# Kernel optimization log

Hardware: AMD Instinct MI355X
Metric: run time of the kernel (lower is better)

## Reference

```python
import jax, jax.numpy as jnp
import numpy as np

SOFTPLUS_MIN = 1e-10
SOFTPLUS_MAX = 10000.0


def setup_inputs() -> dict:
    key = jax.random.key(0)
    k1, k2, k3, k4, k5 = jax.random.split(key, 5)
    N, M, D, S = 8192, 4096, 512, 16
    x = jax.random.normal(k1, (N, D), dtype=jnp.float32)
    y = jax.random.normal(k2, (M, D), dtype=jnp.float32)
    sample_x = jax.random.uniform(k3, (N, S), dtype=jnp.float32)
    sample_y = jax.random.uniform(k4, (M, S), dtype=jnp.float32)
    scale = jax.random.uniform(k5, (S,), dtype=jnp.float32)
    cutoff = jnp.full((1,), 0.1, dtype=jnp.float32)
    phi = jnp.ones((1,), dtype=jnp.float32)
    return {"x": x, "y": y, "sample_x": sample_x, "sample_y": sample_y,
            "scale": scale, "cutoff": cutoff, "phi": phi}


def reference(x, y, sample_x, sample_y, scale, cutoff, phi):
    # pairwise squared distances via norm trick: d[i,j] = |x_i|^2 + |y_j|^2 - 2 x_i.y_j
    sq_x = jnp.sum(x * x, axis=-1, keepdims=True)            # [N,1]
    sq_y = jnp.sum(y * y, axis=-1, keepdims=True).T          # [1,M]
    dot = jnp.matmul(x, y.T)                                 # [N,M]
    d = sq_x + sq_y - 2.0 * dot
    # learned per-sample lengthscales (fixed_scale=False branch)
    scale_x = jnp.clip(jax.nn.softplus(sample_x @ scale[:, None]), SOFTPLUS_MIN, SOFTPLUS_MAX)  # [N,1]
    scale_y = jnp.clip(jax.nn.softplus(sample_y @ scale[:, None]), SOFTPLUS_MIN, SOFTPLUS_MAX)  # [M,1]
    scale_xy = jnp.sqrt(jnp.matmul(scale_x, scale_y.T))      # [N,M] (rank-1 outer product)
    res = 1.0 / (1.0 + d / scale_xy)
    # cutoff.mean() > 0 is statically true for our cutoff=0.1, so mask is always applied
    cut_mask = jax.nn.sigmoid(phi[0] * (res - jnp.clip(cutoff, 0.0, 1000.0)))
    return res * cut_mask
```

## Files before the change

kernel.cpp:

```cpp
#include <hip/hip_runtime.h>
#include <hip/hip_bf16.h>
#include <math.h>

#define N_ROWS 8192
#define M_ROWS 4096
#define DDIM   512
#define SDIM   16

#define BM 128
#define BN 128
#define BK 64

typedef __attribute__((ext_vector_type(8))) __bf16 bf16x8;
typedef __attribute__((ext_vector_type(4))) float f32x4;

__device__ __forceinline__ unsigned short f2bf_rne(float f) {
  unsigned u = __float_as_uint(f);
  u += 0x7fffu + ((u >> 16) & 1u);
  return (unsigned short)(u >> 16);
}

__device__ __forceinline__ void load_lds16(const void* g, void* l) {
  __builtin_amdgcn_global_load_lds(
      (const __attribute__((address_space(1))) void*)g,
      (__attribute__((address_space(3))) void*)l, 16, 0, 0);
}

__global__ __launch_bounds__(256) void prep_kernel(
    const float* __restrict__ x, const float* __restrict__ y,
    const float* __restrict__ samp_x, const float* __restrict__ samp_y,
    const float* __restrict__ scale,
    ushort* __restrict__ xb, ushort* __restrict__ yb,
    float* __restrict__ sqx, float* __restrict__ sqy,
    float* __restrict__ ssx, float* __restrict__ ssy)
{
  int row = blockIdx.x;
  const float* src; const float* samp; ushort* dst; float* sqo; float* sso;
  if (row < N_ROWS) {
    src = x + (size_t)row * DDIM; samp = samp_x + (size_t)row * SDIM;
    dst = xb + (size_t)row * DDIM; sqo = sqx + row; sso = ssx + row;
  } else {
    int r = row - N_ROWS;
    src = y + (size_t)r * DDIM; samp = samp_y + (size_t)r * SDIM;
    dst = yb + (size_t)r * DDIM; sqo = sqy + r; sso = ssy + r;
  }
  int tid = threadIdx.x;
  float2 v = ((const float2*)src)[tid];
  ushort2 b;
  b.x = f2bf_rne(v.x);
  b.y = f2bf_rne(v.y);
  ((ushort2*)dst)[tid] = b;
  float ss = v.x * v.x + v.y * v.y;
  #pragma unroll
  for (int off = 32; off > 0; off >>= 1) ss += __shfl_down(ss, off, 64);
  __shared__ float red[4];
  if ((tid & 63) == 0) red[tid >> 6] = ss;
  __syncthreads();
  if (tid == 0) {
    float tot = red[0] + red[1] + red[2] + red[3];
    *sqo = tot;
    float acc = 0.f;
    #pragma unroll
    for (int s = 0; s < SDIM; s++) acc += samp[s] * scale[s];
    float sp = (acc > 15.f) ? acc : log1pf(expf(acc));
    sp = fminf(fmaxf(sp, 1e-10f), 10000.f);
    *sso = sqrtf(sp);
  }
}

__global__ __launch_bounds__(256, 2) void cauchy_gemm(
    const ushort* __restrict__ xb, const ushort* __restrict__ yb,
    const float* __restrict__ sqx, const float* __restrict__ sqy,
    const float* __restrict__ ssx, const float* __restrict__ ssy,
    const float* __restrict__ cutoff, const float* __restrict__ phi,
    float* __restrict__ out)
{
  __shared__ ushort As[BM * BK];
  __shared__ ushort Bs[BN * BK];
  const int tid = threadIdx.x;
  const int lane = tid & 63;
  const int w = tid >> 6;
  const int wr = w >> 1, wc = w & 1;
  const int l15 = lane & 15, l16 = lane >> 4;

  const size_t aBase = (size_t)blockIdx.x * BM * DDIM;
  const size_t bBase = (size_t)blockIdx.y * BN * DDIM;

  f32x4 acc[4][4];
  #pragma unroll
  for (int a = 0; a < 4; a++)
    #pragma unroll
    for (int b = 0; b < 4; b++)
      acc[a][b] = (f32x4)(0.f);

  for (int k0 = 0; k0 < DDIM; k0 += BK) {
    #pragma unroll
    for (int c = 0; c < 4; c++) {
      int idx = c * 256 + tid;
      int row = idx >> 3;
      int g = idx & 7;
      int sg = g ^ (row & 7);
      load_lds16(xb + aBase + (size_t)row * DDIM + k0 + sg * 8, As + idx * 8);
      load_lds16(yb + bBase + (size_t)row * DDIM + k0 + sg * 8, Bs + idx * 8);
    }
    __syncthreads();

    #pragma unroll
    for (int kk = 0; kk < 2; kk++) {
      bf16x8 af[4], bfr[4];
      #pragma unroll
      for (int a = 0; a < 4; a++) {
        int row = wr * 64 + a * 16 + l15;
        int gran = kk * 4 + l16;
        int off = row * BK + ((gran ^ (row & 7)) << 3);
        af[a] = *(const bf16x8*)((const char*)As + (size_t)off * 2);
      }
      #pragma unroll
      for (int b = 0; b < 4; b++) {
        int col = wc * 64 + b * 16 + l15;
        int gran = kk * 4 + l16;
        int off = col * BK + ((gran ^ (col & 7)) << 3);
        bfr[b] = *(const bf16x8*)((const char*)Bs + (size_t)off * 2);
      }
      #pragma unroll
      for (int a = 0; a < 4; a++)
        #pragma unroll
        for (int b = 0; b < 4; b++)
          acc[a][b] = __builtin_amdgcn_mfma_f32_16x16x32_bf16(af[a], bfr[b], acc[a][b], 0, 0, 0);
    }
    __syncthreads();
  }

  const float cut_c = fminf(fmaxf(cutoff[0], 0.f), 1000.f);
  const float ph = phi[0];
  const int rowBase = blockIdx.x * BM + wr * 64;
  const int colBase = blockIdx.y * BN + wc * 64;

  float sq_i[4][4], sx_i[4][4];
  #pragma unroll
  for (int a = 0; a < 4; a++)
    #pragma unroll
    for (int r = 0; r < 4; r++) {
      int i = rowBase + a * 16 + l16 * 4 + r;
      sq_i[a][r] = sqx[i];
      sx_i[a][r] = ssx[i];
    }
  float sq_j[4], sy_j[4];
  #pragma unroll
  for (int b = 0; b < 4; b++) {
    int j = colBase + b * 16 + l15;
    sq_j[b] = sqy[j];
    sy_j[b] = ssy[j];
  }

  const float L2E = 1.4426950408889634f;
  #pragma unroll
  for (int a = 0; a < 4; a++)
    #pragma unroll
    for (int b = 0; b < 4; b++)
      #pragma unroll
      for (int r = 0; r < 4; r++) {
        int i = rowBase + a * 16 + l16 * 4 + r;
        int j = colBase + b * 16 + l15;
        float dot = acc[a][b][r];
        float d = sq_i[a][r] + sq_j[b] - 2.f * dot;
        float s = sx_i[a][r] * sy_j[b];
        float res = s * __builtin_amdgcn_rcpf(s + d);
        float t = ph * (res - cut_c);
        float u = __builtin_amdgcn_exp2f(-t * L2E);
        float cm = __builtin_amdgcn_rcpf(1.f + u);
        out[(size_t)i * M_ROWS + j] = res * cm;
      }
}

extern "C" void kernel_launch(void* const* d_in, const int* in_sizes, int n_in,
                              void* d_out, int out_size, void* d_ws, size_t ws_size,
                              hipStream_t stream) {
  const float* x       = (const float*)d_in[0];
  const float* y       = (const float*)d_in[1];
  const float* samp_x  = (const float*)d_in[2];
  const float* samp_y  = (const float*)d_in[3];
  const float* scale   = (const float*)d_in[4];
  const float* cutoff  = (const float*)d_in[5];
  const float* phi     = (const float*)d_in[6];
  float* out = (float*)d_out;

  char* p = (char*)d_ws;
  ushort* xb = (ushort*)p; p += (size_t)N_ROWS * DDIM * 2;
  ushort* yb = (ushort*)p; p += (size_t)M_ROWS * DDIM * 2;
  float* sqx = (float*)p;  p += (size_t)N_ROWS * 4;
  float* sqy = (float*)p;  p += (size_t)M_ROWS * 4;
  float* ssx = (float*)p;  p += (size_t)N_ROWS * 4;
  float* ssy = (float*)p;  p += (size_t)M_ROWS * 4;

  prep_kernel<<<N_ROWS + M_ROWS, 256, 0, stream>>>(
      x, y, samp_x, samp_y, scale, xb, yb, sqx, sqy, ssx, ssy);

  dim3 grid(N_ROWS / BM, M_ROWS / BN);
  cauchy_gemm<<<grid, 256, 0, stream>>>(
      xb, yb, sqx, sqy, ssx, ssy, cutoff, phi, out);
}
```

Before: 61.42 us.

## Double-buffer GEMM LDS loads, swizzle block order, streamline epilogue with nontemporal stores

The GEMM k-loop now uses BK=32 with double-buffered LDS, so the global-to-LDS loads for the next step are issued while MFMAs run on the current buffer. One barrier per step replaces the two it had before. The launch becomes a 1D grid with a block-index remap that groups tiles for L2 reuse, and occupancy is raised to 3 blocks per CU. The epilogue folds the constants into FMAs, loads row data per a-block to cut register pressure, and writes output with nontemporal stores. The added occupancy and double buffering could spill registers or shrink the tiles' per-step work.

```diff
diff --git a/kernel.cpp b/kernel.cpp
--- a/kernel.cpp
+++ b/kernel.cpp
@@ -9,7 +9,8 @@
 
 #define BM 128
 #define BN 128
-#define BK 64
+#define BKS 32
+#define NSTEP (DDIM / BKS)
 
 typedef __attribute__((ext_vector_type(8))) __bf16 bf16x8;
 typedef __attribute__((ext_vector_type(4))) float f32x4;
@@ -68,83 +69,94 @@
   }
 }
 
-__global__ __launch_bounds__(256, 2) void cauchy_gemm(
+__global__ __launch_bounds__(256, 3) void cauchy_gemm(
     const ushort* __restrict__ xb, const ushort* __restrict__ yb,
     const float* __restrict__ sqx, const float* __restrict__ sqy,
     const float* __restrict__ ssx, const float* __restrict__ ssy,
     const float* __restrict__ cutoff, const float* __restrict__ phi,
     float* __restrict__ out)
 {
-  __shared__ ushort As[BM * BK];
-  __shared__ ushort Bs[BN * BK];
-  const int tid = threadIdx.x;
+  __shared__ ushort As[2][BM * BKS];
+  __shared__ ushort Bs[2][BN * BKS];
+
+  const int tid  = threadIdx.x;
   const int lane = tid & 63;
-  const int w = tid >> 6;
+  const int w    = tid >> 6;
   const int wr = w >> 1, wc = w & 1;
   const int l15 = lane & 15, l16 = lane >> 4;
 
-  const size_t aBase = (size_t)blockIdx.x * BM * DDIM;
-  const size_t bBase = (size_t)blockIdx.y * BN * DDIM;
+  const int bid  = blockIdx.x;
+  const int sbid = (bid & 7) * 256 + (bid >> 3);
+  const int bx = sbid >> 5;
+  const int by = sbid & 31;
+
+  const int i0 = tid, i1 = tid + 256;
+  const int r0 = i0 >> 2, r1 = i1 >> 2;
+  const int c0 = (i0 & 3) ^ ((r0 >> 1) & 3);
+  const int c1 = (i1 & 3) ^ ((r1 >> 1) & 3);
+  const ushort* aS0 = xb + (size_t)(bx * BM + r0) * DDIM + c0 * 8;
+  const ushort* aS1 = xb + (size_t)(bx * BM + r1) * DDIM + c1 * 8;
+  const ushort* bS0 = yb + (size_t)(by * BN + r0) * DDIM + c0 * 8;
+  const ushort* bS1 = yb + (size_t)(by * BN + r1) * DDIM + c1 * 8;
+  const int d0 = i0 * 8, d1 = i1 * 8;
+
+  int aoff[4], boff[4];
+  #pragma unroll
+  for (int a = 0; a < 4; a++) {
+    int row = wr * 64 + a * 16 + l15;
+    aoff[a] = row * BKS + ((l16 ^ ((row >> 1) & 3)) << 3);
+  }
+  #pragma unroll
+  for (int b = 0; b < 4; b++) {
+    int col = wc * 64 + b * 16 + l15;
+    boff[b] = col * BKS + ((l16 ^ ((col >> 1) & 3)) << 3);
+  }
 
   f32x4 acc[4][4];
   #pragma unroll
   for (int a = 0; a < 4; a++)
     #pragma unroll
-    for (int b = 0; b < 4; b++)
-      acc[a][b] = (f32x4)(0.f);
-
-  for (int k0 = 0; k0 < DDIM; k0 += BK) {
-    #pragma unroll
-    for (int c = 0; c < 4; c++) {
-      int idx = c * 256 + tid;
-      int row = idx >> 3;
-      int g = idx & 7;
-      int sg = g ^ (row & 7);
-      load_lds16(xb + aBase + (size_t)row * DDIM + k0 + sg * 8, As + idx * 8);
-      load_lds16(yb + bBase + (size_t)row * DDIM + k0 + sg * 8, Bs + idx * 8);
+    for (int b = 0; b < 4; b++) acc[a][b] = (f32x4)(0.f);
+
+  load_lds16(aS0, &As[0][d0]); load_lds16(aS1, &As[0][d1]);
+  load_lds16(bS0, &Bs[0][d0]); load_lds16(bS1, &Bs[0][d1]);
+  asm volatile("s_waitcnt vmcnt(0)" ::: "memory");
+  __builtin_amdgcn_s_barrier();
+
+  #pragma unroll
+  for (int s = 0; s < NSTEP; ++s) {
+    const int cur = s & 1, nxt = cur ^ 1;
+    if (s + 1 < NSTEP) {
+      const int ko = (s + 1) * BKS;
+      load_lds16(aS0 + ko, &As[nxt][d0]);
+      load_lds16(aS1 + ko, &As[nxt][d1]);
+      load_lds16(bS0 + ko, &Bs[nxt][d0]);
+      load_lds16(bS1 + ko, &Bs[nxt][d1]);
     }
-    __syncthreads();
-
-    #pragma unroll
-    for (int kk = 0; kk < 2; kk++) {
-      bf16x8 af[4], bfr[4];
+    bf16x8 af[4], bf[4];
+    #pragma unroll
+    for (int a = 0; a < 4; a++) af[a] = *(const bf16x8*)&As[cur][aoff[a]];
+    #pragma unroll
+    for (int b = 0; b < 4; b++) bf[b] = *(const bf16x8*)&Bs[cur][boff[b]];
+
+    __builtin_amdgcn_s_setprio(1);
+    #pragma unroll
+    for (int a = 0; a < 4; a++)
       #pragma unroll
-      for (int a = 0; a < 4; a++) {
-        int row = wr * 64 + a * 16 + l15;
-        int gran = kk * 4 + l16;
-        int off = row * BK + ((gran ^ (row & 7)) << 3);
-        af[a] = *(const bf16x8*)((const char*)As + (size_t)off * 2);
-      }
-      #pragma unroll
-      for (int b = 0; b < 4; b++) {
-        int col = wc * 64 + b * 16 + l15;
-        int gran = kk * 4 + l16;
-        int off = col * BK + ((gran ^ (col & 7)) << 3);
-        bfr[b] = *(const bf16x8*)((const char*)Bs + (size_t)off * 2);
-      }
-      #pragma unroll
-      for (int a = 0; a < 4; a++)
-        #pragma unroll
-        for (int b = 0; b < 4; b++)
-          acc[a][b] = __builtin_amdgcn_mfma_f32_16x16x32_bf16(af[a], bfr[b], acc[a][b], 0, 0, 0);
-    }
-    __syncthreads();
+      for (int b = 0; b < 4; b++)
+        acc[a][b] = __builtin_amdgcn_mfma_f32_16x16x32_bf16(af[a], bf[b], acc[a][b], 0, 0, 0);
+    __builtin_amdgcn_s_setprio(0);
+
+    asm volatile("s_waitcnt vmcnt(0)" ::: "memory");
+    __builtin_amdgcn_s_barrier();
   }
 
   const float cut_c = fminf(fmaxf(cutoff[0], 0.f), 1000.f);
-  const float ph = phi[0];
-  const int rowBase = blockIdx.x * BM + wr * 64;
-  const int colBase = blockIdx.y * BN + wc * 64;
-
-  float sq_i[4][4], sx_i[4][4];
-  #pragma unroll
-  for (int a = 0; a < 4; a++)
-    #pragma unroll
-    for (int r = 0; r < 4; r++) {
-      int i = rowBase + a * 16 + l16 * 4 + r;
-      sq_i[a][r] = sqx[i];
-      sx_i[a][r] = ssx[i];
-    }
+  const float q  = phi[0] * 1.4426950408889634f;
+  const float qc = q * cut_c;
+  const int rowBase = bx * BM + wr * 64;
+  const int colBase = by * BN + wc * 64;
+
   float sq_j[4], sy_j[4];
   #pragma unroll
   for (int b = 0; b < 4; b++) {
@@ -152,25 +164,32 @@
     sq_j[b] = sqy[j];
     sy_j[b] = ssy[j];
   }
-
-  const float L2E = 1.4426950408889634f;
-  #pragma unroll
-  for (int a = 0; a < 4; a++)
-    #pragma unroll
-    for (int b = 0; b < 4; b++)
+  #pragma unroll
+  for (int a = 0; a < 4; a++) {
+    float sq_i[4], sx_i[4];
+    #pragma unroll
+    for (int r = 0; r < 4; r++) {
+      int i = rowBase + a * 16 + l16 * 4 + r;
+      sq_i[r] = sqx[i];
+      sx_i[r] = ssx[i];
+    }
+    #pragma unroll
+    for (int b = 0; b < 4; b++) {
       #pragma unroll
       for (int r = 0; r < 4; r++) {
         int i = rowBase + a * 16 + l16 * 4 + r;
         int j = colBase + b * 16 + l15;
         float dot = acc[a][b][r];
-        float d = sq_i[a][r] + sq_j[b] - 2.f * dot;
-        float s = sx_i[a][r] * sy_j[b];
+        float d = __builtin_fmaf(-2.f, dot, sq_i[r] + sq_j[b]);
+        float s = sx_i[r] * sy_j[b];
         float res = s * __builtin_amdgcn_rcpf(s + d);
-        float t = ph * (res - cut_c);
-        float u = __builtin_amdgcn_exp2f(-t * L2E);
-        float cm = __builtin_amdgcn_rcpf(1.f + u);
-        out[(size_t)i * M_ROWS + j] = res * cm;
+        float earg = __builtin_fmaf(-q, res, qc);
+        float u = __builtin_amdgcn_exp2f(earg);
+        float o = res * __builtin_amdgcn_rcpf(1.f + u);
+        __builtin_nontemporal_store(o, out + (size_t)i * M_ROWS + j);
       }
+    }
+  }
 }
 
 extern "C" void kernel_launch(void* const* d_in, const int* in_sizes, int n_in,
@@ -196,7 +215,6 @@
   prep_kernel<<<N_ROWS + M_ROWS, 256, 0, stream>>>(
       x, y, samp_x, samp_y, scale, xb, yb, sqx, sqy, ssx, ssy);
 
-  dim3 grid(N_ROWS / BM, M_ROWS / BN);
-  cauchy_gemm<<<grid, 256, 0, stream>>>(
+  cauchy_gemm<<<(N_ROWS / BM) * (M_ROWS / BN), 256, 0, stream>>>(
       xb, yb, sqx, sqy, ssx, ssy, cutoff, phi, out);
 }
```

After: 78.28 us. 1.27x slower.
